# Optimization experiments

Measured on AMD Instinct MI355X. Metric: run time of the kernel, lower is better.

## Reference

```python
import jax, jax.numpy as jnp
import numpy as np

NUM_REL = 7
EPS = 1e-5
N, E = 30000, 480000
D_IN, D_H = 21, 512


def _bn(x, g, b):
    # BatchNorm1d over nodes (training-mode batch statistics, biased var like torch)
    mu = x.mean(axis=0)
    var = x.var(axis=0)
    return (x - mu) * jax.lax.rsqrt(var + EPS) * g + b


def _conv(x, src, seg_idx, lin_w, lin_b, self_w, self_b, bn_g, bn_b):
    # GeometricRelationalGraphConv: gather src features, scatter-add per (dst, relation)
    d = x.shape[1]
    msg = x[src]                                                   # (E, d)
    upd = jax.ops.segment_sum(msg, seg_idx, num_segments=N * NUM_REL)
    upd = upd.reshape(N, NUM_REL * d)                              # (N, 7*d)
    out = upd @ lin_w.T + lin_b + x @ self_w.T + self_b            # linear + self-loop
    out = _bn(out, bn_g, bn_b)                                     # conv-internal BN
    return jax.nn.relu(out)


def setup_inputs() -> dict:
    key = jax.random.key(0)
    ks = jax.random.split(key, 16)
    inp = {
        "x": jax.random.normal(ks[0], (N, D_IN), dtype=jnp.float32),
        "src": jax.random.randint(ks[1], (E,), 0, N, dtype=jnp.int32),
        "dst": jax.random.randint(ks[2], (E,), 0, N, dtype=jnp.int32),
        "rel": jax.random.randint(ks[3], (E,), 0, NUM_REL, dtype=jnp.int32),
    }
    dims = [(D_IN, D_H), (D_H, D_H), (D_H, D_H)]
    k = 4
    for i, (din, dout) in enumerate(dims):
        inp[f"lin_w{i}"] = jax.random.normal(ks[k], (dout, NUM_REL * din), dtype=jnp.float32) * 0.05
        inp[f"self_w{i}"] = jax.random.normal(ks[k + 1], (dout, din), dtype=jnp.float32) * 0.05
        k += 2
        inp[f"lin_b{i}"] = jnp.zeros((dout,), jnp.float32)
        inp[f"self_b{i}"] = jnp.zeros((dout,), jnp.float32)
        inp[f"bn1_g{i}"] = jnp.ones((dout,), jnp.float32)
        inp[f"bn1_b{i}"] = jnp.zeros((dout,), jnp.float32)
        inp[f"bn2_g{i}"] = jnp.ones((dout,), jnp.float32)
        inp[f"bn2_b{i}"] = jnp.zeros((dout,), jnp.float32)
    return inp


def reference(x, src, dst, rel,
              lin_w0, lin_b0, self_w0, self_b0, bn1_g0, bn1_b0, bn2_g0, bn2_b0,
              lin_w1, lin_b1, self_w1, self_b1, bn1_g1, bn1_b1, bn2_g1, bn2_b1,
              lin_w2, lin_b2, self_w2, self_b2, bn1_g2, bn1_b2, bn2_g2, bn2_b2):
    seg_idx = dst * NUM_REL + rel                                  # (E,)
    layers = [
        (lin_w0, lin_b0, self_w0, self_b0, bn1_g0, bn1_b0, bn2_g0, bn2_b0),
        (lin_w1, lin_b1, self_w1, self_b1, bn1_g1, bn1_b1, bn2_g1, bn2_b1),
        (lin_w2, lin_b2, self_w2, self_b2, bn1_g2, bn1_b2, bn2_g2, bn2_b2),
    ]
    hiddens = []
    h = x
    for lw, lb, sw, sb, g1, b1, g2, b2 in layers:
        h = _conv(h, src, seg_idx, lw, lb, sw, sb, g1, b1)
        h = _bn(h, g2, b2)                                         # GearNet outer BN
        hiddens.append(h)
    return jnp.concatenate(hiddens, axis=-1)                      # (N, 3*512) concat_hidden
```

## Files before the change

### kernel.cpp

```cpp
#include <hip/hip_runtime.h>

#define NN   30000
#define NE   480000
#define NR   7
#define NSEG (NN*NR)
#define DH   512
#define DIN  21
#define EPSB 1e-5f
#define BK   32
#define KSEG 3584
#define CHMAX 15360

typedef __attribute__((ext_vector_type(8))) short bf16x8;
typedef __attribute__((ext_vector_type(8))) unsigned short u16x8;
typedef __attribute__((ext_vector_type(4))) float f32x4;
typedef unsigned short ushortT;

static inline size_t align256(size_t x){ return (x + 255) & ~(size_t)255; }

__device__ inline float bf2f(ushortT u){
    unsigned int i = ((unsigned int)u) << 16; float f; __builtin_memcpy(&f, &i, 4); return f;
}
__device__ inline ushortT f2bf(float f){
    unsigned int i; __builtin_memcpy(&i, &f, 4);
    unsigned int r = i + 0x7FFFu + ((i >> 16) & 1u);
    return (ushortT)(r >> 16);
}

__device__ inline void load_lds16(const ushortT* g, ushortT* l){
    __builtin_amdgcn_global_load_lds((const __attribute__((address_space(1))) unsigned int*)g,
                                     (__attribute__((address_space(3))) unsigned int*)l,
                                     16, 0, 0);
}


__global__ void hist_k(const int* __restrict__ dst, const int* __restrict__ rel,
                       int* __restrict__ counts){
    int e = blockIdx.x*256 + threadIdx.x;
    if (e < NE) atomicAdd(&counts[dst[e]*NR + rel[e]], 1);
}

__global__ void scan1_k(const int* __restrict__ counts, int* __restrict__ bsum){
    __shared__ int sd[256];
    int t = threadIdx.x;
    int base = blockIdx.x*1024 + t*4;
    int s = 0;
#pragma unroll
    for (int i = 0; i < 4; i++){ int idx = base + i; if (idx < NSEG) s += counts[idx]; }
    sd[t] = s; __syncthreads();
    for (int off = 128; off > 0; off >>= 1){
        if (t < off) sd[t] += sd[t+off];
        __syncthreads();
    }
    if (t == 0) bsum[blockIdx.x] = sd[0];
}

__global__ void scan2_k(int* __restrict__ bsum, int nb, int* __restrict__ seg_start){
    __shared__ int sd[256];
    int t = threadIdx.x;
    int v = (t < nb) ? bsum[t] : 0;
    sd[t] = v; __syncthreads();
    for (int off = 1; off < 256; off <<= 1){
        int x = sd[t];
        if (t >= off) x += sd[t-off];
        __syncthreads();
        sd[t] = x; __syncthreads();
    }
    if (t < nb) bsum[t] = (t == 0) ? 0 : sd[t-1];
    if (t == 0) seg_start[NSEG] = NE;
}

__global__ void scan3_k(const int* __restrict__ counts, const int* __restrict__ bsum,
                        int* __restrict__ seg_start){
    __shared__ int sd[256];
    int t = threadIdx.x;
    int base = blockIdx.x*1024 + t*4;
    int v[4]; int s = 0;
#pragma unroll
    for (int i = 0; i < 4; i++){ int idx = base + i; v[i] = (idx < NSEG) ? counts[idx] : 0; s += v[i]; }
    sd[t] = s; __syncthreads();
    for (int off = 1; off < 256; off <<= 1){
        int x = sd[t];
        if (t >= off) x += sd[t-off];
        __syncthreads();
        sd[t] = x; __syncthreads();
    }
    int excl = sd[t] - s + bsum[blockIdx.x];
#pragma unroll
    for (int i = 0; i < 4; i++){
        int idx = base + i;
        if (idx < NSEG){ seg_start[idx] = excl; excl += v[i]; }
    }
}

__global__ void scatter_k(const int* __restrict__ src, const int* __restrict__ dst,
                          const int* __restrict__ rel, const int* __restrict__ seg_start,
                          int* __restrict__ cursor, int* __restrict__ src_sorted){
    int e = blockIdx.x*256 + threadIdx.x;
    if (e < NE){
        int s = dst[e]*NR + rel[e];
        int pos = seg_start[s] + atomicAdd(&cursor[s], 1);
        src_sorted[pos] = src[e];
    }
}


__global__ void segsum21b_k(const float* __restrict__ x0,
                            const int* __restrict__ seg_start, const int* __restrict__ src_sorted,
                            ushortT* __restrict__ Acat){
    int n = blockIdx.x;
    int t = threadIdx.x;
    ushortT* arow = Acat + (long)n*192;
    if (t < DIN){
        int sb = n*NR;
        int e0 = seg_start[sb];
#pragma unroll
        for (int r = 0; r < NR; r++){
            int e1 = seg_start[sb + r + 1];
            float a = 0.f;
            for (int e = e0; e < e1; e++) a += x0[(long)src_sorted[e]*DIN + t];
            e0 = e1;
            arow[r*DIN + t] = f2bf(a);
        }
        arow[7*DIN + t] = f2bf(x0[(long)n*DIN + t]);
    }
    if (t >= 40) arow[168 + (t - 40)] = 0;
}


__global__ __launch_bounds__(256)
void segsum_wave_k(const ushortT* __restrict__ hbf,
                   const int* __restrict__ seg_start, const int* __restrict__ src_sorted,
                   ushortT* __restrict__ Acat, int c0, int cn){
    int wid = (blockIdx.x*256 + threadIdx.x) >> 6;
    if (wid >= cn) return;
    const int n = c0 + wid;
    const int lane = (threadIdx.x & 63);
    const int co = lane*8;

    int sb[8];
#pragma unroll
    for (int i = 0; i < 8; i++) sb[i] = seg_start[n*NR + i];

    ushortT* arow = Acat + (long)wid*KSEG + co;
#pragma unroll
    for (int r = 0; r < NR; r++){
        float a[8];
#pragma unroll
        for (int j = 0; j < 8; j++) a[j] = 0.f;
        int e = sb[r], e1 = sb[r+1];
        for (; e + 1 < e1; e += 2){
            u16x8 v0 = *reinterpret_cast<const u16x8*>(hbf + (long)src_sorted[e]*DH + co);
            u16x8 v1 = *reinterpret_cast<const u16x8*>(hbf + (long)src_sorted[e+1]*DH + co);
#pragma unroll
            for (int j = 0; j < 8; j++) a[j] += bf2f((ushortT)v0[j]) + bf2f((ushortT)v1[j]);
        }
        if (e < e1){
            u16x8 v = *reinterpret_cast<const u16x8*>(hbf + (long)src_sorted[e]*DH + co);
#pragma unroll
            for (int j = 0; j < 8; j++) a[j] += bf2f((ushortT)v[j]);
        }
        u16x8 o;
#pragma unroll
        for (int j = 0; j < 8; j++) o[j] = f2bf(a[j]);
        *reinterpret_cast<u16x8*>(arow + r*DH) = o;
    }
}


__global__ void convw_k(const float* __restrict__ lw, const float* __restrict__ sw,
                        int d, int Kp, ushortT* __restrict__ Wc){
    int i = blockIdx.x*256 + threadIdx.x;
    if (i < DH*Kp){
        int n = i / Kp, k = i % Kp;
        float v;
        if (k < 7*d)      v = lw[(long)n*7*d + k];
        else if (k < 8*d) v = sw[(long)n*d + (k - 7*d)];
        else              v = 0.f;
        Wc[i] = f2bf(v);
    }
}


__global__ __launch_bounds__(256)
void gemm_mfma_k(const ushortT* __restrict__ A, int lda, int ntA,
                 const ushortT* __restrict__ hbase, int M,
                 const ushortT* __restrict__ W, int ldw,
                 const float* __restrict__ b1, const float* __restrict__ b2,
                 float* __restrict__ C, int nt, float* __restrict__ sums){
    __shared__ ushortT As[2][128*BK];
    __shared__ ushortT Bs[2][128*BK];
    const int t    = threadIdx.x;
    const int bm   = blockIdx.y*128;
    const int bn   = blockIdx.x*128;
    const int w    = t >> 6;
    const int lane = t & 63;

    int f0 = w*128 + lane, f1 = f0 + 64;
    const int ar0 = min(bm + (f0 >> 2), M-1), ac0 = (f0 & 3)*8;
    const int ar1 = min(bm + (f1 >> 2), M-1), ac1 = (f1 & 3)*8;
    const int br0 = bn + (f0 >> 2), br1 = bn + (f1 >> 2);
    const int d0 = (w*128 +  0)*8;
    const int d1 = (w*128 + 64)*8;

    f32x4 acc[4][4];
#pragma unroll
    for (int m = 0; m < 4; m++)
#pragma unroll
        for (int n = 0; n < 4; n++) acc[m][n] = (f32x4){0.f,0.f,0.f,0.f};

    const int wm = w >> 1, wn = w & 1;
    const int r = lane & 15, hi = lane >> 4;

    auto stage = [&](int kt, int b){
        const ushortT* p0;
        const ushortT* p1;
        if (kt < ntA){
            p0 = A + (long)ar0*lda + kt*BK + ac0;
            p1 = A + (long)ar1*lda + kt*BK + ac1;
        } else {
            int k0 = (kt - ntA)*BK;
            p0 = hbase + (long)ar0*DH + k0 + ac0;
            p1 = hbase + (long)ar1*DH + k0 + ac1;
        }
        load_lds16(p0, &As[b][d0]);
        load_lds16(p1, &As[b][d1]);
        load_lds16(W + (long)br0*ldw + kt*BK + ac0, &Bs[b][d0]);
        load_lds16(W + (long)br1*ldw + kt*BK + ac1, &Bs[b][d1]);
    };

    stage(0, 0);

    for (int kt = 0; kt < nt; ++kt){
        __syncthreads();
        if (kt + 1 < nt) stage(kt + 1, (kt + 1) & 1);
        int buf = kt & 1;
        bf16x8 af[4], bfr[4];
#pragma unroll
        for (int m = 0; m < 4; m++)
            af[m] = *reinterpret_cast<const bf16x8*>(&As[buf][(wm*64 + m*16 + r)*BK + hi*8]);
#pragma unroll
        for (int n = 0; n < 4; n++)
            bfr[n] = *reinterpret_cast<const bf16x8*>(&Bs[buf][(wn*64 + n*16 + r)*BK + hi*8]);
#pragma unroll
        for (int m = 0; m < 4; m++)
#pragma unroll
            for (int n = 0; n < 4; n++)
                acc[m][n] = __builtin_amdgcn_mfma_f32_16x16x32_bf16(af[m], bfr[n], acc[m][n], 0, 0, 0);
    }

#pragma unroll
    for (int n = 0; n < 4; n++){
        int col = bn + wn*64 + n*16 + r;
        float bb = b1[col] + b2[col];
        float s = 0.f, s2 = 0.f;
#pragma unroll
        for (int m = 0; m < 4; m++){
            int row = bm + wm*64 + m*16 + hi*4;
#pragma unroll
            for (int q = 0; q < 4; q++){
                if (row + q < M){
                    float v = acc[m][n][q] + bb;
                    C[(long)(row + q)*DH + col] = v;
                    s += v; s2 = fmaf(v, v, s2);
                }
            }
        }
        s  += __shfl_xor(s, 16);  s  += __shfl_xor(s, 32);
        s2 += __shfl_xor(s2, 16); s2 += __shfl_xor(s2, 32);
        if (hi == 0){
            atomicAdd(&sums[col], s);
            atomicAdd(&sums[DH + col], s2);
        }
    }
}


__global__ void finalize_k(const float* __restrict__ sums, const float* __restrict__ g,
                           const float* __restrict__ b, float* __restrict__ ac){
    int c = blockIdx.x*256 + threadIdx.x;
    if (c < DH){
        float mu  = sums[c] * (1.f/NN);
        float var = sums[DH + c] * (1.f/NN) - mu*mu;
        var = fmaxf(var, 0.f);
        float a = g[c] * rsqrtf(var + EPSB);
        ac[c]      = a;
        ac[DH + c] = fmaf(-mu, a, b[c]);
    }
}

__global__ void bnrelu_k(float* __restrict__ buf, int M, const float* __restrict__ ac,
                         float* __restrict__ sums2){
    int col = blockIdx.x*256 + threadIdx.x;
    int r0 = blockIdx.y*128;
    int r1 = min(r0 + 128, M);
    float a = ac[col], c = ac[DH + col];
    float s = 0.f, s2 = 0.f;
    for (int r = r0; r < r1; r++){
        long idx = (long)r*DH + col;
        float y = fmaxf(fmaf(a, buf[idx], c), 0.f);
        buf[idx] = y;
        s += y; s2 = fmaf(y, y, s2);
    }
    atomicAdd(&sums2[col], s);
    atomicAdd(&sums2[DH + col], s2);
}

__global__ void bn2write_k(const float* __restrict__ buf, const float* __restrict__ ac,
                           float* __restrict__ out, ushortT* __restrict__ hbf, int layer){
    long i = (long)blockIdx.x*256 + threadIdx.x;
    if (i < (long)NN*DH){
        int r = (int)(i >> 9);
        int c = (int)(i & 511);
        float h = fmaf(ac[c], buf[i], ac[DH + c]);
        out[(long)r*(3*DH) + layer*DH + c] = h;
        hbf[i] = f2bf(h);
    }
}


extern "C" void kernel_launch(void* const* d_in, const int* in_sizes, int n_in,
                              void* d_out, int out_size, void* d_ws, size_t ws_size,
                              hipStream_t stream){
    const float* x0  = (const float*)d_in[0];
    const int*   src = (const int*)d_in[1];
    const int*   dst = (const int*)d_in[2];
    const int*   rel = (const int*)d_in[3];
    const float* lin_w[3]  = {(const float*)d_in[4],  (const float*)d_in[12], (const float*)d_in[20]};
    const float* self_w[3] = {(const float*)d_in[5],  (const float*)d_in[13], (const float*)d_in[21]};
    const float* lin_b[3]  = {(const float*)d_in[6],  (const float*)d_in[14], (const float*)d_in[22]};
    const float* self_b[3] = {(const float*)d_in[7],  (const float*)d_in[15], (const float*)d_in[23]};
    const float* bn1_g[3]  = {(const float*)d_in[8],  (const float*)d_in[16], (const float*)d_in[24]};
    const float* bn1_b[3]  = {(const float*)d_in[9],  (const float*)d_in[17], (const float*)d_in[25]};
    const float* bn2_g[3]  = {(const float*)d_in[10], (const float*)d_in[18], (const float*)d_in[26]};
    const float* bn2_b[3]  = {(const float*)d_in[11], (const float*)d_in[19], (const float*)d_in[27]};

    char* ws = (char*)d_ws;
    size_t off = 0;
    auto alloc = [&](size_t bytes)->char*{ char* p = ws + off; off = align256(off + bytes); return p; };

    int*     counts     = (int*)alloc((size_t)NSEG*4);
    int*     cursor     = (int*)alloc((size_t)NSEG*4);
    int*     seg_start  = (int*)alloc((size_t)(NSEG+1)*4);
    int*     bsum       = (int*)alloc(1024*4);
    int*     src_sorted = (int*)alloc((size_t)NE*4);
    float*   stats      = (float*)alloc((size_t)8*DH*4);
    float*   sums1 = stats;            float* sums2 = stats + 2*DH;
    float*   ac1   = stats + 4*DH;     float* ac2   = stats + 6*DH;
    float*   outbuf = (float*)alloc((size_t)NN*DH*4);
    ushortT* hbf    = (ushortT*)alloc((size_t)NN*DH*2);
    ushortT* Wcat   = (ushortT*)alloc((size_t)DH*4096*2);
    ushortT* Acat0  = (ushortT*)alloc((size_t)NN*192*2);

    size_t remain = (ws_size > off) ? (ws_size - off) : 0;
    long max_nodes = (long)(remain / ((size_t)KSEG*2));
    int chunk = (int)((max_nodes > CHMAX) ? CHMAX : max_nodes);
    chunk &= ~127;
    if (chunk < 128) chunk = 128;
    ushortT* Acat = (ushortT*)(ws + off);

    hipMemsetAsync(counts, 0, (size_t)NSEG*4, stream);
    hipMemsetAsync(cursor, 0, (size_t)NSEG*4, stream);
    hist_k<<<(NE+255)/256, 256, 0, stream>>>(dst, rel, counts);
    int nb = (NSEG + 1023)/1024;
    scan1_k<<<nb, 256, 0, stream>>>(counts, bsum);
    scan2_k<<<1, 256, 0, stream>>>(bsum, nb, seg_start);
    scan3_k<<<nb, 256, 0, stream>>>(counts, bsum, seg_start);
    scatter_k<<<(NE+255)/256, 256, 0, stream>>>(src, dst, rel, seg_start, cursor, src_sorted);

    const int MB = (NN + 127)/128;

    for (int layer = 0; layer < 3; layer++){
        int d  = (layer == 0) ? DIN : DH;
        int Kp = (layer == 0) ? 192 : 8*DH;
        convw_k<<<(DH*Kp + 255)/256, 256, 0, stream>>>(lin_w[layer], self_w[layer], d, Kp, Wcat);
        hipMemsetAsync(stats, 0, (size_t)4*DH*4, stream);

        if (layer == 0){
            segsum21b_k<<<NN, 64, 0, stream>>>(x0, seg_start, src_sorted, Acat0);
            gemm_mfma_k<<<dim3(4, MB), 256, 0, stream>>>(
                Acat0, 192, 6, Acat0, NN, Wcat, 192,
                lin_b[layer], self_b[layer], outbuf, 6, sums1);
        } else {
            for (int c0 = 0; c0 < NN; c0 += chunk){
                int cn = (NN - c0 < chunk) ? (NN - c0) : chunk;
                segsum_wave_k<<<(cn + 3)/4, 256, 0, stream>>>(
                    hbf, seg_start, src_sorted, Acat, c0, cn);
                gemm_mfma_k<<<dim3(4, (cn + 127)/128), 256, 0, stream>>>(
                    Acat, KSEG, 112, hbf + (long)c0*DH, cn, Wcat, 4096,
                    lin_b[layer], self_b[layer],
                    outbuf + (long)c0*DH, 128, sums1);
            }
        }

        finalize_k<<<2, 256, 0, stream>>>(sums1, bn1_g[layer], bn1_b[layer], ac1);
        bnrelu_k<<<dim3(2, (NN+127)/128), 256, 0, stream>>>(outbuf, NN, ac1, sums2);
        finalize_k<<<2, 256, 0, stream>>>(sums2, bn2_g[layer], bn2_b[layer], ac2);
        bn2write_k<<<((long)NN*DH + 255)/256, 256, 0, stream>>>(outbuf, ac2, (float*)d_out, hbf, layer);
    }
}
```

Measured before the change: 972.0 us.

## Triple-buffer GEMM LDS staging and remap blocks across XCDs

The MFMA GEMM moves from double to triple buffering of the A/B tiles in LDS, prefetching two K-steps ahead. It replaces the full __syncthreads with an explicit vmcnt wait plus barrier, so more global-to-LDS loads stay in flight. The grid also becomes 1D, with block ids remapped so that consecutive tiles sharing A rows land on the same XCD for better L2 reuse. The cost is 50% more LDS per block, which may lower occupancy, and the hand-written waitcnt count depends on exactly four loads per stage.

```diff
diff --git a/kernel.cpp b/kernel.cpp
--- a/kernel.cpp
+++ b/kernel.cpp
@@ -188,11 +188,17 @@
                  const ushortT* __restrict__ W, int ldw,
                  const float* __restrict__ b1, const float* __restrict__ b2,
                  float* __restrict__ C, int nt, float* __restrict__ sums){
-    __shared__ ushortT As[2][128*BK];
-    __shared__ ushortT Bs[2][128*BK];
+    __shared__ ushortT As[3][128*BK];
+    __shared__ ushortT Bs[3][128*BK];
     const int t    = threadIdx.x;
-    const int bm   = blockIdx.y*128;
-    const int bn   = blockIdx.x*128;
+
+    const int nwg = gridDim.x;
+    int q = nwg >> 3, rmd = nwg & 7;
+    int xcd = blockIdx.x & 7, slot = blockIdx.x >> 3;
+    int l = xcd*q + min(xcd, rmd) + slot;
+    const int bm = (l >> 2)*128;
+    const int bn = (l & 3)*128;
+
     const int w    = t >> 6;
     const int lane = t & 63;
 
@@ -230,11 +236,15 @@
     };
 
     stage(0, 0);
+    stage(1, 1);
 
     for (int kt = 0; kt < nt; ++kt){
-        __syncthreads();
-        if (kt + 1 < nt) stage(kt + 1, (kt + 1) & 1);
-        int buf = kt & 1;
+        if (kt + 1 < nt) asm volatile("s_waitcnt vmcnt(4)" ::: "memory");
+        else             asm volatile("s_waitcnt vmcnt(0)" ::: "memory");
+        __builtin_amdgcn_s_barrier();
+        __builtin_amdgcn_sched_barrier(0);
+        if (kt + 2 < nt) stage(kt + 2, (kt + 2) % 3);
+        const int buf = kt % 3;
         bf16x8 af[4], bfr[4];
 #pragma unroll
         for (int m = 0; m < 4; m++)
@@ -258,10 +268,10 @@
         for (int m = 0; m < 4; m++){
             int row = bm + wm*64 + m*16 + hi*4;
 #pragma unroll
-            for (int q = 0; q < 4; q++){
-                if (row + q < M){
-                    float v = acc[m][n][q] + bb;
-                    C[(long)(row + q)*DH + col] = v;
+            for (int q2 = 0; q2 < 4; q2++){
+                if (row + q2 < M){
+                    float v = acc[m][n][q2] + bb;
+                    C[(long)(row + q2)*DH + col] = v;
                     s += v; s2 = fmaf(v, v, s2);
                 }
             }
@@ -378,7 +388,7 @@
 
         if (layer == 0){
             segsum21b_k<<<NN, 64, 0, stream>>>(x0, seg_start, src_sorted, Acat0);
-            gemm_mfma_k<<<dim3(4, MB), 256, 0, stream>>>(
+            gemm_mfma_k<<<MB*4, 256, 0, stream>>>(
                 Acat0, 192, 6, Acat0, NN, Wcat, 192,
                 lin_b[layer], self_b[layer], outbuf, 6, sums1);
         } else {
@@ -386,7 +396,7 @@
                 int cn = (NN - c0 < chunk) ? (NN - c0) : chunk;
                 segsum_wave_k<<<(cn + 3)/4, 256, 0, stream>>>(
                     hbf, seg_start, src_sorted, Acat, c0, cn);
-                gemm_mfma_k<<<dim3(4, (cn + 127)/128), 256, 0, stream>>>(
+                gemm_mfma_k<<<((cn + 127)/128)*4, 256, 0, stream>>>(
                     Acat, KSEG, 112, hbf + (long)c0*DH, cn, Wcat, 4096,
                     lin_b[layer], self_b[layer],
                     outbuf + (long)c0*DH, 128, sums1);
```

New measurement: 959.5 us. Within noise of the previous version (-1.3%).
